# Kernel optimization log

Measured on AMD Instinct MI355X. Metric: run time of the kernel, lower is better.

The kernel has to match this reference:

```python
import jax, jax.numpy as jnp
import numpy as np

EMB = 256
HEADS = 8
D_HEAD = EMB // HEADS


def apply_rope(x):
    # x: [B, H, T, D] (interleaved-pair RoPE, matching the torch source)
    T, D = x.shape[-2], x.shape[-1]
    freqs = 10000.0 ** (-jnp.arange(0, D, 2, dtype=jnp.float32) / D)  # [D/2]
    angles = jnp.arange(T, dtype=jnp.float32)[:, None] * freqs[None, :]  # [T, D/2]
    sin = jnp.repeat(jnp.sin(angles), 2, axis=1)  # [T, D]
    cos = jnp.repeat(jnp.cos(angles), 2, axis=1)  # [T, D]
    x1 = x[..., 0::2]
    x2 = x[..., 1::2]
    rotated = jnp.stack((-x2, x1), axis=-1).reshape(x.shape)  # interleave (-x2, x1)
    return x * cos + rotated * sin


def setup_inputs() -> dict:
    key = jax.random.key(0)
    k1, k2, k3, k4, k5 = jax.random.split(key, 5)
    B, T = 8, 2048
    x = jax.random.normal(k1, (B, T, EMB), dtype=jnp.float32)
    s = 1.0 / np.sqrt(EMB)
    # Linear weights stored as [in, out] (torch weight.T), y = x @ W + b
    Wqkv = jax.random.uniform(k2, (EMB, 3 * EMB), minval=-s, maxval=s, dtype=jnp.float32)
    bqkv = jax.random.uniform(k3, (3 * EMB,), minval=-s, maxval=s, dtype=jnp.float32)
    Wout = jax.random.uniform(k4, (EMB, EMB), minval=-s, maxval=s, dtype=jnp.float32)
    bout = jax.random.uniform(k5, (EMB,), minval=-s, maxval=s, dtype=jnp.float32)
    return {"x": x, "Wqkv": Wqkv, "bqkv": bqkv, "Wout": Wout, "bout": bout}


def reference(x, Wqkv, bqkv, Wout, bout):
    B, T, E = x.shape
    H, Dh = HEADS, D_HEAD
    qkv = x @ Wqkv + bqkv  # [B, T, 3E]
    qkv = qkv.reshape(B, T, 3, H, Dh).transpose(2, 0, 3, 1, 4)  # [3, B, H, T, Dh]
    q, k, v = qkv[0], qkv[1], qkv[2]
    q = apply_rope(q)
    k = apply_rope(k)
    scores = jnp.einsum('bhtd,bhsd->bhts', q, k) / np.sqrt(Dh)  # [B, H, T, T]
    causal = jnp.triu(jnp.ones((T, T), dtype=bool), k=1)
    scores = jnp.where(causal, -jnp.inf, scores)
    attn = jax.nn.softmax(scores, axis=-1)
    out = jnp.einsum('bhts,bhsd->bthd', attn, v).reshape(B, T, E)
    return out @ Wout + bout
```

## Files before the change

kernel.cpp:

```cpp
#include <hip/hip_runtime.h>
#include <hip/hip_bf16.h>
#include <math.h>

typedef __hip_bfloat16 bf16;
using s8v = __attribute__((ext_vector_type(8))) short;
using f4v = __attribute__((ext_vector_type(4))) float;

__device__ __forceinline__ float bfb2f(unsigned short u) {
    return __uint_as_float(((unsigned int)u) << 16);
}
__device__ __forceinline__ unsigned short f2bfb(float f) {
    unsigned int u = __float_as_uint(f);
    unsigned int r = (u + 0x7fffu + ((u >> 16) & 1u)) >> 16;
    return (unsigned short)r;
}
__device__ __forceinline__ unsigned int packbf2_rne(float a, float b) {
    return (unsigned int)f2bfb(a) | ((unsigned int)f2bfb(b) << 16);
}
__device__ __forceinline__ unsigned int packbf2(float a, float b) {
    return __builtin_amdgcn_perm(__float_as_uint(b) + 0x8000u,
                                 __float_as_uint(a) + 0x8000u,
                                 0x07060302u);
}

__device__ __forceinline__ void gload_lds16(const void* g, void* l) {
    __builtin_amdgcn_global_load_lds(
        (const __attribute__((address_space(1))) unsigned int*)g,
        (__attribute__((address_space(3))) unsigned int*)l, 16, 0, 0);
}

__device__ __forceinline__ int sniff_fp32(const void* p, int tid, int* s_flag)
{
    if (tid == 0) *s_flag = 0;
    __syncthreads();
    const uint4* u = (const uint4*)p;
    int local = 0;
    #pragma unroll
    for (int i = 0; i < 4; i++) {
        const uint4 v = u[i * 256 + tid];
        if ((v.x & 0x7F80u) == 0x7F80u) local = 1;
        if ((v.y & 0x7F80u) == 0x7F80u) local = 1;
        if ((v.z & 0x7F80u) == 0x7F80u) local = 1;
        if ((v.w & 0x7F80u) == 0x7F80u) local = 1;
    }
    if (local) atomicOr(s_flag, 1);
    __syncthreads();
    return *s_flag;
}

__global__ __launch_bounds__(256)
void k_prep(const void* __restrict__ x, const void* __restrict__ Wqkv,
            const void* __restrict__ bqkv, const void* __restrict__ Wout,
            const void* __restrict__ bout,
            bf16* __restrict__ wqkvT, bf16* __restrict__ woutT,
            float* __restrict__ bq_f, float* __restrict__ bo_f,
            bf16* __restrict__ xb)
{
    __shared__ int sf;
    const int bid = blockIdx.x;
    const int tid = threadIdx.x;
    if (bid < 768) {
        const int f = sniff_fp32(Wqkv, tid, &sf);
        unsigned short v = f ? f2bfb(((const float*)Wqkv)[(size_t)tid * 768 + bid])
                             : ((const unsigned short*)Wqkv)[(size_t)tid * 768 + bid];
        ((unsigned short*)wqkvT)[(size_t)bid * 256 + tid] = v;
        if (bid < 12) {
            const int i = bid * 256 + tid;
            bq_f[i] = f ? ((const float*)bqkv)[i]
                        : bfb2f(((const unsigned short*)bqkv)[i]);
        }
    } else if (bid < 1024) {
        const int n = bid - 768;
        const int f = sniff_fp32(Wout, tid, &sf);
        unsigned short v = f ? f2bfb(((const float*)Wout)[(size_t)tid * 256 + n])
                             : ((const unsigned short*)Wout)[(size_t)tid * 256 + n];
        ((unsigned short*)woutT)[(size_t)n * 256 + tid] = v;
        if (n == 0)
            bo_f[tid] = f ? ((const float*)bout)[tid]
                          : bfb2f(((const unsigned short*)bout)[tid]);
    } else {
        const int f = sniff_fp32(x, tid, &sf);
        if (f) {
            const size_t cb = (size_t)(bid - 1024) * 4096;
            #pragma unroll
            for (int i = 0; i < 4; i++) {
                const size_t e = cb + (size_t)i * 1024 + tid * 4;
                const float4 v = *(const float4*)((const float*)x + e);
                ushort4 o4;
                o4.x = f2bfb(v.x);
                o4.y = f2bfb(v.y);
                o4.z = f2bfb(v.z);
                o4.w = f2bfb(v.w);
                *(ushort4*)((unsigned short*)xb + e) = o4;
            }
        } else {
            const size_t base = (size_t)(bid - 1024) * 4096 + (size_t)tid * 16;
            const uint4* xu = (const uint4*)((const unsigned short*)x + base);
            uint4* dp = (uint4*)((unsigned short*)xb + base);
            dp[0] = xu[0];
            dp[1] = xu[1];
        }
    }
}

__global__ __launch_bounds__(256)
void k_qkv_rope(const bf16* __restrict__ xb, const bf16* __restrict__ wqkvT,
                const float* __restrict__ bq_f,
                bf16* __restrict__ q_ws, bf16* __restrict__ k_ws,
                bf16* __restrict__ vT_ws)
{
    __shared__ __align__(16) unsigned short Bls[4][8][512];
    __shared__ __align__(16) unsigned short Tls[4][1536];

    const int tid = threadIdx.x;
    const int bx = blockIdx.x;
    const int by = blockIdx.y;
    const int n0 = bx * 64;

    const int w    = tid >> 6;
    const int lane = tid & 63;
    const int col  = lane & 15;
    const int quad = lane >> 4;
    const int which = n0 >> 8;
    const int b     = (by * 128) >> 11;
    unsigned short* Tw = Tls[w];

    #pragma unroll
    for (int kk = 0; kk < 8; kk++)
        gload_lds16((const unsigned short*)wqkvT +
                        (size_t)(n0 + w * 16 + col) * 256 + kk * 32 + quad * 8,
                    &Bls[w][kk][0]);
    __syncthreads();

    const int T0 = by * 128 + w * 32;

    f4v acc[2][4] = {{{0.f,0.f,0.f,0.f}, {0.f,0.f,0.f,0.f},
                      {0.f,0.f,0.f,0.f}, {0.f,0.f,0.f,0.f}},
                     {{0.f,0.f,0.f,0.f}, {0.f,0.f,0.f,0.f},
                      {0.f,0.f,0.f,0.f}, {0.f,0.f,0.f,0.f}}};

    #pragma unroll
    for (int kk = 0; kk < 8; kk++) {
        const s8v av0 = *(const s8v*)((const unsigned short*)xb +
                        (size_t)(T0 + col) * 256 + kk * 32 + quad * 8);
        const s8v av1 = *(const s8v*)((const unsigned short*)xb +
                        (size_t)(T0 + 16 + col) * 256 + kk * 32 + quad * 8);
        #pragma unroll
        for (int c = 0; c < 4; c++) {
            const s8v bv = *(const s8v*)&Bls[c][kk][lane * 8];
            acc[0][c] = __builtin_amdgcn_mfma_f32_16x16x32_bf16(av0, bv, acc[0][c], 0, 0, 0);
            acc[1][c] = __builtin_amdgcn_mfma_f32_16x16x32_bf16(av1, bv, acc[1][c], 0, 0, 0);
        }
    }

    #pragma unroll
    for (int g = 0; g < 2; g++) {
        const int t_base = ((by * 128) & 2047) + w * 32 + g * 16;

        if (which == 2) {
            #pragma unroll
            for (int c = 0; c < 4; c++) {
                const int nl = c * 16 + col;
                const float bias = bq_f[n0 + nl];
                uint2 ww;
                ww.x = packbf2_rne(acc[g][c][0] + bias, acc[g][c][1] + bias);
                ww.y = packbf2_rne(acc[g][c][2] + bias, acc[g][c][3] + bias);
                *(uint2*)(Tw + nl * 24 + quad * 4) = ww;
            }
            const int ng = n0 + lane;
            const int h = (ng & 255) >> 5;
            const int d = ng & 31;
            const s8v t0 = *(const s8v*)&Tw[lane * 24];
            const s8v t1 = *(const s8v*)&Tw[lane * 24 + 8];
            unsigned short* dp = (unsigned short*)vT_ws +
                ((size_t)(b * 8 + h) * 32 + d) * 2048 + t_base;
            *(s8v*)dp = t0;
            *(s8v*)(dp + 8) = t1;
        } else {
            #pragma unroll
            for (int c = 0; c < 4; c++) {
                const int nl = c * 16 + col;
                const int d = (n0 + nl) & 31;
                const float bias = bq_f[n0 + nl];
                const float frev = __expf(-0.28782314f * (float)(d & ~1))
                                 * 0.15915494309189535f;
                #pragma unroll
                for (int r = 0; r < 4; r++) {
                    const float v = acc[g][c][r] + bias;
                    const float vp = __shfl_xor(v, 1);
                    const int t = t_base + quad * 4 + r;
                    float rev = (float)t * frev;
                    rev -= floorf(rev);
                    const float ang = rev * 6.283185307179586f;
                    const float sn = __sinf(ang);
                    const float cs = __cosf(ang);
                    float o = (d & 1) ? (v * cs + vp * sn)
                                      : (v * cs - vp * sn);
                    if (which == 0) o *= 0.17677669529663687f;
                    Tw[(quad * 4 + r) * 80 + nl] = f2bfb(o);
                }
            }
            const int row = lane >> 2;
            const int ch  = lane & 3;
            const int ng  = n0 + ch * 16;
            const int h   = (ng & 255) >> 5;
            const int d   = ng & 31;
            const int t   = t_base + row;
            const s8v t0 = *(const s8v*)&Tw[row * 80 + ch * 16];
            const s8v t1 = *(const s8v*)&Tw[row * 80 + ch * 16 + 8];
            unsigned short* dp = (unsigned short*)(which ? k_ws : q_ws) +
                ((size_t)(b * 8 + h) * 2048 + t) * 32 + d;
            *(s8v*)dp = t0;
            *(s8v*)(dp + 8) = t1;
        }
    }
}

__global__ __launch_bounds__(256, 4)
void k_attn(const bf16* __restrict__ q_ws, const bf16* __restrict__ k_ws,
            const bf16* __restrict__ vT_ws, bf16* __restrict__ ctx)
{
    __shared__ __align__(16) unsigned short KVls[2][8][512];
    __shared__ __align__(16) unsigned short Pls[4][16 * 72];

    const int tid  = threadIdx.x;
    const int w    = tid >> 6;
    const int lane = tid & 63;
    const int col  = lane & 15;
    const int quad = lane >> 4;

    const int idx = blockIdx.x;
    const int bh  = idx & 63;
    const int mb  = 31 - (idx >> 6);
    const int T0  = mb * 64 + w * 16;

    const bf16* qb = q_ws  + (size_t)bh * 65536;
    const bf16* kb = k_ws  + (size_t)bh * 65536;
    const bf16* vb = vT_ws + (size_t)bh * 65536;

    const bf16* kg = kb + (size_t)(w * 16 + col) * 32 + quad * 8;
    const bf16* vg = vb + (size_t)(col + (w & 1) * 16) * 2048
                        + (w >> 1) * 32 + quad * 8;

    const s8v qa = *(const s8v*)(qb + (size_t)(T0 + col) * 32 + quad * 8);

    f4v o0 = {0.f,0.f,0.f,0.f}, o1 = {0.f,0.f,0.f,0.f};
    float lp[4] = {0.f,0.f,0.f,0.f};

    unsigned short* Pw = Pls[w];

    gload_lds16(kg, &KVls[0][w][0]);
    gload_lds16(vg, &KVls[0][4 + w][0]);
    __syncthreads();

    int cur = 0;
    for (int kt = 0; kt <= mb; kt++) {
        const int s0 = kt * 64;

        if (kt < mb) {
            gload_lds16(kg + (size_t)(kt + 1) * 2048, &KVls[cur ^ 1][w][0]);
            gload_lds16(vg + (kt + 1) * 64,           &KVls[cur ^ 1][4 + w][0]);
        }

        const s8v kf0 = *(const s8v*)&KVls[cur][0][lane * 8];
        const s8v kf1 = *(const s8v*)&KVls[cur][1][lane * 8];
        const s8v kf2 = *(const s8v*)&KVls[cur][2][lane * 8];
        const s8v kf3 = *(const s8v*)&KVls[cur][3][lane * 8];
        const s8v v00 = *(const s8v*)&KVls[cur][4][lane * 8];
        const s8v v10 = *(const s8v*)&KVls[cur][5][lane * 8];
        const s8v v01 = *(const s8v*)&KVls[cur][6][lane * 8];
        const s8v v11 = *(const s8v*)&KVls[cur][7][lane * 8];

        const f4v z = {0.f, 0.f, 0.f, 0.f};
        f4v s[4];
        s[0] = __builtin_amdgcn_mfma_f32_16x16x32_bf16(kf0, qa, z, 0, 0, 0);
        s[1] = __builtin_amdgcn_mfma_f32_16x16x32_bf16(kf1, qa, z, 0, 0, 0);
        s[2] = __builtin_amdgcn_mfma_f32_16x16x32_bf16(kf2, qa, z, 0, 0, 0);
        s[3] = __builtin_amdgcn_mfma_f32_16x16x32_bf16(kf3, qa, z, 0, 0, 0);

        if (kt == mb) {
            #pragma unroll
            for (int c = 0; c < 4; c++) {
                const int sbase = s0 + c * 16 + quad * 4;
                #pragma unroll
                for (int r = 0; r < 4; r++)
                    if (sbase + r > T0 + col) s[c][r] = -INFINITY;
            }
        }

        #pragma unroll
        for (int c = 0; c < 4; c++) {
            const float p0 = __expf(s[c][0]);
            const float p1 = __expf(s[c][1]);
            const float p2 = __expf(s[c][2]);
            const float p3 = __expf(s[c][3]);
            lp[0] += p0; lp[1] += p1; lp[2] += p2; lp[3] += p3;
            uint2 ww;
            ww.x = packbf2(p0, p1);
            ww.y = packbf2(p2, p3);
            *(uint2*)(Pw + col * 72 + c * 16 + quad * 4) = ww;
        }

        {
            const s8v pb0 = *(const s8v*)&Pw[col * 72 + quad * 8];
            const s8v pb1 = *(const s8v*)&Pw[col * 72 + 32 + quad * 8];
            o0 = __builtin_amdgcn_mfma_f32_16x16x32_bf16(pb0, v00, o0, 0, 0, 0);
            o1 = __builtin_amdgcn_mfma_f32_16x16x32_bf16(pb0, v10, o1, 0, 0, 0);
            o0 = __builtin_amdgcn_mfma_f32_16x16x32_bf16(pb1, v01, o0, 0, 0, 0);
            o1 = __builtin_amdgcn_mfma_f32_16x16x32_bf16(pb1, v11, o1, 0, 0, 0);
        }

        __syncthreads();
        cur ^= 1;
    }

    float rs = lp[0] + lp[1] + lp[2] + lp[3];
    rs += __shfl_xor(rs, 16);
    rs += __shfl_xor(rs, 32);

    const int b = bh >> 3;
    const int h = bh & 7;
    unsigned short* cp = (unsigned short*)ctx;
    #pragma unroll
    for (int r = 0; r < 4; r++) {
        const float inv = 1.0f / __shfl(rs, quad * 4 + r);
        const float e0 = o0[r] * inv;
        const float e1 = o1[r] * inv;
        const int t = T0 + quad * 4 + r;
        unsigned short* dst = cp + (size_t)(b * 2048 + t) * 256 + h * 32;
        dst[col]      = f2bfb(e0);
        dst[col + 16] = f2bfb(e1);
    }
}

__global__ __launch_bounds__(256)
void k_outproj(const bf16* __restrict__ ctx, const bf16* __restrict__ woutT,
               const float* __restrict__ bo_f, float* __restrict__ out)
{
    __shared__ __align__(16) unsigned short Bls[4][8][512];

    const int tid = threadIdx.x;
    const int bx = blockIdx.x;
    const int by = blockIdx.y;
    const int n0 = bx * 64;

    const int w    = tid >> 6;
    const int lane = tid & 63;
    const int col  = lane & 15;
    const int quad = lane >> 4;

    #pragma unroll
    for (int kk = 0; kk < 8; kk++)
        gload_lds16((const unsigned short*)woutT +
                        (size_t)(n0 + w * 16 + col) * 256 + kk * 32 + quad * 8,
                    &Bls[w][kk][0]);
    __syncthreads();

    const int T0 = by * 128 + w * 32;

    f4v acc[2][4] = {{{0.f,0.f,0.f,0.f}, {0.f,0.f,0.f,0.f},
                      {0.f,0.f,0.f,0.f}, {0.f,0.f,0.f,0.f}},
                     {{0.f,0.f,0.f,0.f}, {0.f,0.f,0.f,0.f},
                      {0.f,0.f,0.f,0.f}, {0.f,0.f,0.f,0.f}}};

    #pragma unroll
    for (int kk = 0; kk < 8; kk++) {
        const s8v av0 = *(const s8v*)((const unsigned short*)ctx +
                        (size_t)(T0 + col) * 256 + kk * 32 + quad * 8);
        const s8v av1 = *(const s8v*)((const unsigned short*)ctx +
                        (size_t)(T0 + 16 + col) * 256 + kk * 32 + quad * 8);
        #pragma unroll
        for (int c = 0; c < 4; c++) {
            const s8v bv = *(const s8v*)&Bls[c][kk][lane * 8];
            acc[0][c] = __builtin_amdgcn_mfma_f32_16x16x32_bf16(av0, bv, acc[0][c], 0, 0, 0);
            acc[1][c] = __builtin_amdgcn_mfma_f32_16x16x32_bf16(av1, bv, acc[1][c], 0, 0, 0);
        }
    }

    #pragma unroll
    for (int g = 0; g < 2; g++) {
        #pragma unroll
        for (int c = 0; c < 4; c++) {
            const int n = n0 + c * 16 + col;
            const float bias = bo_f[n];
            #pragma unroll
            for (int r = 0; r < 4; r++)
                out[(size_t)(T0 + g * 16 + quad * 4 + r) * 256 + n] =
                    acc[g][c][r] + bias;
        }
    }
}

extern "C" void kernel_launch(void* const* d_in, const int* in_sizes, int n_in,
                              void* d_out, int out_size, void* d_ws, size_t ws_size,
                              hipStream_t stream)
{
    const void* x    = d_in[0];
    const void* Wqkv = d_in[1];
    const void* bqkv = d_in[2];
    const void* Wout = d_in[3];
    const void* bout = d_in[4];
    float* out = (float*)d_out;

    const size_t NQ = (size_t)8 * 8 * 2048 * 32;
    bf16* q_ws   = (bf16*)d_ws;
    bf16* k_ws   = q_ws + NQ;
    bf16* vT_ws  = k_ws + NQ;
    bf16* ctx    = vT_ws + NQ;
    bf16* xb     = ctx;
    bf16* wqkvT  = ctx + NQ;
    bf16* woutT  = wqkvT + (size_t)768 * 256;
    float* bq_f  = (float*)(woutT + (size_t)256 * 256);
    float* bo_f  = bq_f + 3072;

    k_prep    <<<2048,          256, 0, stream>>>(x, Wqkv, bqkv, Wout, bout,
                                                  wqkvT, woutT, bq_f, bo_f, xb);
    k_qkv_rope<<<dim3(12, 128), 256, 0, stream>>>(xb, wqkvT, bq_f,
                                                  q_ws, k_ws, vT_ws);
    k_attn    <<<2048,          256, 0, stream>>>(q_ws, k_ws, vT_ws, ctx);
    k_outproj <<<dim3(4, 128),  256, 0, stream>>>(ctx, woutT, bo_f, out);
}
```

Baseline: 152.1 us.

## Give each attention wave two query row-tiles, halving waves per block

The attention kernel now runs 2 waves per block instead of 4, and each wave handles 32 query rows as two 16-row MFMA tiles. Each wave loads two K and two V chunks per step, and the K/V fragments it reads from LDS are reused across both query tiles. This halves LDS fragment reads per query row and cuts the number of waves taking part in each barrier. In exchange it raises register pressure (more accumulators and score tiles) and serialises the two P staging passes through one LDS buffer per wave.

```diff
diff --git a/kernel.cpp b/kernel.cpp
--- a/kernel.cpp
+++ b/kernel.cpp
@@ -216,12 +216,12 @@
     }
 }
 
-__global__ __launch_bounds__(256, 4)
+__global__ __launch_bounds__(128)
 void k_attn(const bf16* __restrict__ q_ws, const bf16* __restrict__ k_ws,
             const bf16* __restrict__ vT_ws, bf16* __restrict__ ctx)
 {
     __shared__ __align__(16) unsigned short KVls[2][8][512];
-    __shared__ __align__(16) unsigned short Pls[4][16 * 72];
+    __shared__ __align__(16) unsigned short Pls[2][16 * 72];
 
     const int tid  = threadIdx.x;
     const int w    = tid >> 6;
@@ -232,34 +232,45 @@
     const int idx = blockIdx.x;
     const int bh  = idx & 63;
     const int mb  = 31 - (idx >> 6);
-    const int T0  = mb * 64 + w * 16;
+    const int T0  = mb * 64 + w * 32;
 
     const bf16* qb = q_ws  + (size_t)bh * 65536;
     const bf16* kb = k_ws  + (size_t)bh * 65536;
     const bf16* vb = vT_ws + (size_t)bh * 65536;
 
-    const bf16* kg = kb + (size_t)(w * 16 + col) * 32 + quad * 8;
-    const bf16* vg = vb + (size_t)(col + (w & 1) * 16) * 2048
-                        + (w >> 1) * 32 + quad * 8;
-
-    const s8v qa = *(const s8v*)(qb + (size_t)(T0 + col) * 32 + quad * 8);
-
-    f4v o0 = {0.f,0.f,0.f,0.f}, o1 = {0.f,0.f,0.f,0.f};
-    float lp[4] = {0.f,0.f,0.f,0.f};
+    const int c0 = 2 * w, c1 = 2 * w + 1;
+    const bf16* kg0 = kb + (size_t)(c0 * 16 + col) * 32 + quad * 8;
+    const bf16* kg1 = kb + (size_t)(c1 * 16 + col) * 32 + quad * 8;
+    const bf16* vg0 = vb + (size_t)(col + (c0 & 1) * 16) * 2048
+                         + (c0 >> 1) * 32 + quad * 8;
+    const bf16* vg1 = vb + (size_t)(col + (c1 & 1) * 16) * 2048
+                         + (c1 >> 1) * 32 + quad * 8;
+
+    const s8v qa0 = *(const s8v*)(qb + (size_t)(T0 + col) * 32 + quad * 8);
+    const s8v qa1 = *(const s8v*)(qb + (size_t)(T0 + 16 + col) * 32 + quad * 8);
+
+    f4v o00 = {0.f,0.f,0.f,0.f}, o01 = {0.f,0.f,0.f,0.f};
+    f4v o10 = {0.f,0.f,0.f,0.f}, o11 = {0.f,0.f,0.f,0.f};
+    float lp0[4] = {0.f,0.f,0.f,0.f};
+    float lp1[4] = {0.f,0.f,0.f,0.f};
 
     unsigned short* Pw = Pls[w];
 
-    gload_lds16(kg, &KVls[0][w][0]);
-    gload_lds16(vg, &KVls[0][4 + w][0]);
+    gload_lds16(kg0, &KVls[0][c0][0]);
+    gload_lds16(kg1, &KVls[0][c1][0]);
+    gload_lds16(vg0, &KVls[0][4 + c0][0]);
+    gload_lds16(vg1, &KVls[0][4 + c1][0]);
     __syncthreads();
 
     int cur = 0;
     for (int kt = 0; kt <= mb; kt++) {
-        const int s0 = kt * 64;
+        const int stile = kt * 64;
 
         if (kt < mb) {
-            gload_lds16(kg + (size_t)(kt + 1) * 2048, &KVls[cur ^ 1][w][0]);
-            gload_lds16(vg + (kt + 1) * 64,           &KVls[cur ^ 1][4 + w][0]);
+            gload_lds16(kg0 + (size_t)(kt + 1) * 2048, &KVls[cur ^ 1][c0][0]);
+            gload_lds16(kg1 + (size_t)(kt + 1) * 2048, &KVls[cur ^ 1][c1][0]);
+            gload_lds16(vg0 + (kt + 1) * 64,           &KVls[cur ^ 1][4 + c0][0]);
+            gload_lds16(vg1 + (kt + 1) * 64,           &KVls[cur ^ 1][4 + c1][0]);
         }
 
         const s8v kf0 = *(const s8v*)&KVls[cur][0][lane * 8];
@@ -272,64 +283,98 @@
         const s8v v11 = *(const s8v*)&KVls[cur][7][lane * 8];
 
         const f4v z = {0.f, 0.f, 0.f, 0.f};
-        f4v s[4];
-        s[0] = __builtin_amdgcn_mfma_f32_16x16x32_bf16(kf0, qa, z, 0, 0, 0);
-        s[1] = __builtin_amdgcn_mfma_f32_16x16x32_bf16(kf1, qa, z, 0, 0, 0);
-        s[2] = __builtin_amdgcn_mfma_f32_16x16x32_bf16(kf2, qa, z, 0, 0, 0);
-        s[3] = __builtin_amdgcn_mfma_f32_16x16x32_bf16(kf3, qa, z, 0, 0, 0);
+        f4v sA[4], sB[4];
+        sA[0] = __builtin_amdgcn_mfma_f32_16x16x32_bf16(kf0, qa0, z, 0, 0, 0);
+        sA[1] = __builtin_amdgcn_mfma_f32_16x16x32_bf16(kf1, qa0, z, 0, 0, 0);
+        sA[2] = __builtin_amdgcn_mfma_f32_16x16x32_bf16(kf2, qa0, z, 0, 0, 0);
+        sA[3] = __builtin_amdgcn_mfma_f32_16x16x32_bf16(kf3, qa0, z, 0, 0, 0);
+        sB[0] = __builtin_amdgcn_mfma_f32_16x16x32_bf16(kf0, qa1, z, 0, 0, 0);
+        sB[1] = __builtin_amdgcn_mfma_f32_16x16x32_bf16(kf1, qa1, z, 0, 0, 0);
+        sB[2] = __builtin_amdgcn_mfma_f32_16x16x32_bf16(kf2, qa1, z, 0, 0, 0);
+        sB[3] = __builtin_amdgcn_mfma_f32_16x16x32_bf16(kf3, qa1, z, 0, 0, 0);
 
         if (kt == mb) {
             #pragma unroll
             for (int c = 0; c < 4; c++) {
-                const int sbase = s0 + c * 16 + quad * 4;
+                const int sbase = stile + c * 16 + quad * 4;
                 #pragma unroll
-                for (int r = 0; r < 4; r++)
-                    if (sbase + r > T0 + col) s[c][r] = -INFINITY;
+                for (int r = 0; r < 4; r++) {
+                    if (sbase + r > T0 + col)      sA[c][r] = -INFINITY;
+                    if (sbase + r > T0 + 16 + col) sB[c][r] = -INFINITY;
+                }
             }
         }
 
         #pragma unroll
         for (int c = 0; c < 4; c++) {
-            const float p0 = __expf(s[c][0]);
-            const float p1 = __expf(s[c][1]);
-            const float p2 = __expf(s[c][2]);
-            const float p3 = __expf(s[c][3]);
-            lp[0] += p0; lp[1] += p1; lp[2] += p2; lp[3] += p3;
+            const float p0 = __expf(sA[c][0]);
+            const float p1 = __expf(sA[c][1]);
+            const float p2 = __expf(sA[c][2]);
+            const float p3 = __expf(sA[c][3]);
+            lp0[0] += p0; lp0[1] += p1; lp0[2] += p2; lp0[3] += p3;
             uint2 ww;
             ww.x = packbf2(p0, p1);
             ww.y = packbf2(p2, p3);
             *(uint2*)(Pw + col * 72 + c * 16 + quad * 4) = ww;
         }
-
+        {
+            const s8v pa0 = *(const s8v*)&Pw[col * 72 + quad * 8];
+            const s8v pa1 = *(const s8v*)&Pw[col * 72 + 32 + quad * 8];
+            o00 = __builtin_amdgcn_mfma_f32_16x16x32_bf16(pa0, v00, o00, 0, 0, 0);
+            o01 = __builtin_amdgcn_mfma_f32_16x16x32_bf16(pa0, v10, o01, 0, 0, 0);
+            o00 = __builtin_amdgcn_mfma_f32_16x16x32_bf16(pa1, v01, o00, 0, 0, 0);
+            o01 = __builtin_amdgcn_mfma_f32_16x16x32_bf16(pa1, v11, o01, 0, 0, 0);
+        }
+
+        #pragma unroll
+        for (int c = 0; c < 4; c++) {
+            const float p0 = __expf(sB[c][0]);
+            const float p1 = __expf(sB[c][1]);
+            const float p2 = __expf(sB[c][2]);
+            const float p3 = __expf(sB[c][3]);
+            lp1[0] += p0; lp1[1] += p1; lp1[2] += p2; lp1[3] += p3;
+            uint2 ww;
+            ww.x = packbf2(p0, p1);
+            ww.y = packbf2(p2, p3);
+            *(uint2*)(Pw + col * 72 + c * 16 + quad * 4) = ww;
+        }
         {
             const s8v pb0 = *(const s8v*)&Pw[col * 72 + quad * 8];
             const s8v pb1 = *(const s8v*)&Pw[col * 72 + 32 + quad * 8];
-            o0 = __builtin_amdgcn_mfma_f32_16x16x32_bf16(pb0, v00, o0, 0, 0, 0);
-            o1 = __builtin_amdgcn_mfma_f32_16x16x32_bf16(pb0, v10, o1, 0, 0, 0);
-            o0 = __builtin_amdgcn_mfma_f32_16x16x32_bf16(pb1, v01, o0, 0, 0, 0);
-            o1 = __builtin_amdgcn_mfma_f32_16x16x32_bf16(pb1, v11, o1, 0, 0, 0);
+            o10 = __builtin_amdgcn_mfma_f32_16x16x32_bf16(pb0, v00, o10, 0, 0, 0);
+            o11 = __builtin_amdgcn_mfma_f32_16x16x32_bf16(pb0, v10, o11, 0, 0, 0);
+            o10 = __builtin_amdgcn_mfma_f32_16x16x32_bf16(pb1, v01, o10, 0, 0, 0);
+            o11 = __builtin_amdgcn_mfma_f32_16x16x32_bf16(pb1, v11, o11, 0, 0, 0);
         }
 
         __syncthreads();
         cur ^= 1;
     }
 
-    float rs = lp[0] + lp[1] + lp[2] + lp[3];
-    rs += __shfl_xor(rs, 16);
-    rs += __shfl_xor(rs, 32);
+    float rs0 = lp0[0] + lp0[1] + lp0[2] + lp0[3];
+    rs0 += __shfl_xor(rs0, 16);
+    rs0 += __shfl_xor(rs0, 32);
+    float rs1 = lp1[0] + lp1[1] + lp1[2] + lp1[3];
+    rs1 += __shfl_xor(rs1, 16);
+    rs1 += __shfl_xor(rs1, 32);
 
     const int b = bh >> 3;
     const int h = bh & 7;
     unsigned short* cp = (unsigned short*)ctx;
     #pragma unroll
-    for (int r = 0; r < 4; r++) {
-        const float inv = 1.0f / __shfl(rs, quad * 4 + r);
-        const float e0 = o0[r] * inv;
-        const float e1 = o1[r] * inv;
-        const int t = T0 + quad * 4 + r;
-        unsigned short* dst = cp + (size_t)(b * 2048 + t) * 256 + h * 32;
-        dst[col]      = f2bfb(e0);
-        dst[col + 16] = f2bfb(e1);
+    for (int g = 0; g < 2; g++) {
+        const float rs = g ? rs1 : rs0;
+        const int T0g = T0 + g * 16;
+        #pragma unroll
+        for (int r = 0; r < 4; r++) {
+            const float inv = 1.0f / __shfl(rs, quad * 4 + r);
+            const float e0 = (g ? o10[r] : o00[r]) * inv;
+            const float e1 = (g ? o11[r] : o01[r]) * inv;
+            const int t = T0g + quad * 4 + r;
+            unsigned short* dst = cp + (size_t)(b * 2048 + t) * 256 + h * 32;
+            dst[col]      = f2bfb(e0);
+            dst[col + 16] = f2bfb(e1);
+        }
     }
 }
 
@@ -417,6 +462,6 @@
                                                   wqkvT, woutT, bq_f, bo_f, xb);
     k_qkv_rope<<<dim3(12, 128), 256, 0, stream>>>(xb, wqkvT, bq_f,
                                                   q_ws, k_ws, vT_ws);
-    k_attn    <<<2048,          256, 0, stream>>>(q_ws, k_ws, vT_ws, ctx);
+    k_attn    <<<2048,          128, 0, stream>>>(q_ws, k_ws, vT_ws, ctx);
     k_outproj <<<dim3(4, 128),  256, 0, stream>>>(ctx, woutT, bo_f, out);
 }
```

Result: slower. 160.7 us (+5.6%).
